# Kernel tuning notes

Hardware: AMD Instinct MI355X
Metric: run time of the kernel (lower is better)

The kernel has to match this reference:

```python
import jax, jax.numpy as jnp
import numpy as np

B, S, H = 32, 1024, 512
D = 2 * H  # feature dim used by all projections


def setup_inputs() -> dict:
    key = jax.random.key(0)
    ks = jax.random.split(key, 8)
    sc = 1.0 / np.sqrt(D)
    return {
        "h_dec": jax.random.normal(ks[0], (1, B, H), jnp.float32),
        "c_dec": jax.random.normal(ks[1], (1, B, H), jnp.float32),
        "encoder_output": jax.random.normal(ks[2], (B, S, D), jnp.float32),
        "x_padding_masks": jnp.ones((B, S), jnp.float32),
        "coverage_vector": jnp.zeros((B, S), jnp.float32),
        "Wh_w": jax.random.normal(ks[3], (D, D), jnp.float32) * sc,
        "Ws_w": jax.random.normal(ks[4], (D, D), jnp.float32) * sc,
        "Ws_b": jax.random.normal(ks[5], (D,), jnp.float32) * sc,
        "Wc_w": jax.random.normal(ks[6], (D, 1), jnp.float32) * sc,
        "v_w": jax.random.normal(ks[7], (1, D), jnp.float32) * sc,
    }


def reference(h_dec, c_dec, encoder_output, x_padding_masks, coverage_vector,
              Wh_w, Ws_w, Ws_b, Wc_w, v_w):
    # s_t: (B, 1, 2H) -- decoder state, broadcast over seq instead of expand
    s_t = jnp.concatenate([h_dec, c_dec], axis=-1).transpose(1, 0, 2)
    dec_feat = s_t @ Ws_w.T + Ws_b                                  # (B,1,D)
    enc_feat = jnp.einsum('bsd,ed->bse', encoder_output, Wh_w)      # (B,S,D)
    cov_feat = coverage_vector[..., None] * Wc_w[:, 0]              # (B,S,D)
    atten_inputs = enc_feat + dec_feat + cov_feat
    score = jnp.einsum('bsd,d->bs', atten_inputs, v_w[0])           # (B,S)
    w = jax.nn.softmax(score, axis=1) * x_padding_masks
    w = w / jnp.sum(w, axis=1, keepdims=True)                       # renormalize
    context = jnp.einsum('bs,bsd->bd', w, encoder_output)           # (B,2H)
    coverage_new = coverage_vector + w
    return context, w, coverage_new
```

## Files before the change

kernel.cpp:

```cpp
#include <hip/hip_runtime.h>
#include <math.h>

#define B 32
#define S 1024
#define D 1024
#define NCHUNK 32
#define CROWS (S / NCHUNK)
#define WROWS (CROWS / 4)
#define THR 10.0f

#define WS_U      0
#define WS_CSC    1024
#define WS_SCORE  2048
#define WS_ML     (WS_SCORE + B * S)
#define WS_CTX    (WS_ML + B * NCHUNK * 2)

__global__ __launch_bounds__(256) void prep_kernel(
    const float* __restrict__ Wh, const float* __restrict__ Wc,
    const float* __restrict__ v, float* __restrict__ ws) {
    int blk = blockIdx.x, tid = threadIdx.x;
    if (blk == 128) {
        float p = 0.f;
        #pragma unroll
        for (int k = 0; k < 4; ++k) { int i = tid + k * 256; p += v[i] * Wc[i]; }
        __shared__ float red[256];
        red[tid] = p; __syncthreads();
        for (int s = 128; s > 0; s >>= 1) {
            if (tid < s) red[tid] += red[tid + s];
            __syncthreads();
        }
        if (tid == 0) ws[WS_CSC] = red[0];
        return;
    }
    int dchunk = blk >> 5, echunk = blk & 31;
    int d = dchunk * 256 + tid, e0 = echunk * 32;
    float acc = 0.f;
    #pragma unroll 8
    for (int e = e0; e < e0 + 32; ++e)
        acc += v[e] * Wh[e * D + d];
    atomicAdd(&ws[WS_U + d], acc);
}

__global__ __launch_bounds__(256) void fused_kernel(
    const float4* __restrict__ enc4, const float* __restrict__ cov,
    const float* __restrict__ mask, float* __restrict__ ws) {
    int chunk = blockIdx.x, b = blockIdx.y;
    int tid = threadIdx.x, wave = tid >> 6, lane = tid & 63;

    __shared__ float lds_ctx[4][D];
    __shared__ float lds_ml[4][2];

    const float4* u4 = (const float4*)(ws + WS_U);
    float4 uv0 = u4[lane * 4 + 0], uv1 = u4[lane * 4 + 1];
    float4 uv2 = u4[lane * 4 + 2], uv3 = u4[lane * 4 + 3];
    float cscale = ws[WS_CSC];

    float m = -INFINITY, l = 0.f;
    float4 c0 = make_float4(0, 0, 0, 0), c1 = c0, c2 = c0, c3 = c0;

    int s_base = chunk * CROWS + wave * WROWS;
    for (int r = 0; r < WROWS; r += 2) {
        int idxA = b * S + s_base + r;
        int idxB = idxA + 1;
        size_t roA = (size_t)idxA * 256 + lane * 4;
        size_t roB = (size_t)idxB * 256 + lane * 4;
        float4 a0 = enc4[roA + 0], a1 = enc4[roA + 1], a2 = enc4[roA + 2], a3 = enc4[roA + 3];
        float4 b0 = enc4[roB + 0], b1 = enc4[roB + 1], b2 = enc4[roB + 2], b3 = enc4[roB + 3];
        float accA = a0.x * uv0.x + a0.y * uv0.y + a0.z * uv0.z + a0.w * uv0.w
                   + a1.x * uv1.x + a1.y * uv1.y + a1.z * uv1.z + a1.w * uv1.w
                   + a2.x * uv2.x + a2.y * uv2.y + a2.z * uv2.z + a2.w * uv2.w
                   + a3.x * uv3.x + a3.y * uv3.y + a3.z * uv3.z + a3.w * uv3.w;
        float accB = b0.x * uv0.x + b0.y * uv0.y + b0.z * uv0.z + b0.w * uv0.w
                   + b1.x * uv1.x + b1.y * uv1.y + b1.z * uv1.z + b1.w * uv1.w
                   + b2.x * uv2.x + b2.y * uv2.y + b2.z * uv2.z + b2.w * uv2.w
                   + b3.x * uv3.x + b3.y * uv3.y + b3.z * uv3.z + b3.w * uv3.w;
        #pragma unroll
        for (int off = 32; off > 0; off >>= 1) {
            accA += __shfl_xor(accA, off, 64);
            accB += __shfl_xor(accB, off, 64);
        }
        float scA = accA + cov[idxA] * cscale;
        float scB = accB + cov[idxB] * cscale;
        if (lane == 0) {
            ws[WS_SCORE + idxA] = scA;
            ws[WS_SCORE + idxB] = scB;
        }
        float mx = fmaxf(scA, scB);
        if (mx > m + THR) {
            float scl = __expf(m - mx);
            l *= scl;
            c0.x *= scl; c0.y *= scl; c0.z *= scl; c0.w *= scl;
            c1.x *= scl; c1.y *= scl; c1.z *= scl; c1.w *= scl;
            c2.x *= scl; c2.y *= scl; c2.z *= scl; c2.w *= scl;
            c3.x *= scl; c3.y *= scl; c3.z *= scl; c3.w *= scl;
            m = mx;
        }
        float eA = __expf(scA - m) * mask[idxA];
        float eB = __expf(scB - m) * mask[idxB];
        l += eA + eB;
        c0.x += eA * a0.x + eB * b0.x; c0.y += eA * a0.y + eB * b0.y;
        c0.z += eA * a0.z + eB * b0.z; c0.w += eA * a0.w + eB * b0.w;
        c1.x += eA * a1.x + eB * b1.x; c1.y += eA * a1.y + eB * b1.y;
        c1.z += eA * a1.z + eB * b1.z; c1.w += eA * a1.w + eB * b1.w;
        c2.x += eA * a2.x + eB * b2.x; c2.y += eA * a2.y + eB * b2.y;
        c2.z += eA * a2.z + eB * b2.z; c2.w += eA * a2.w + eB * b2.w;
        c3.x += eA * a3.x + eB * b3.x; c3.y += eA * a3.y + eB * b3.y;
        c3.z += eA * a3.z + eB * b3.z; c3.w += eA * a3.w + eB * b3.w;
    }

    {
        float4* lc = (float4*)lds_ctx[wave];
        lc[lane * 4 + 0] = c0; lc[lane * 4 + 1] = c1;
        lc[lane * 4 + 2] = c2; lc[lane * 4 + 3] = c3;
        if (lane == 0) { lds_ml[wave][0] = m; lds_ml[wave][1] = l; }
    }
    __syncthreads();
    {
        float m0 = lds_ml[0][0], m1 = lds_ml[1][0], m2 = lds_ml[2][0], m3 = lds_ml[3][0];
        float mc = fmaxf(fmaxf(m0, m1), fmaxf(m2, m3));
        float f0 = __expf(m0 - mc), f1 = __expf(m1 - mc);
        float f2 = __expf(m2 - mc), f3 = __expf(m3 - mc);
        float lc = lds_ml[0][1] * f0 + lds_ml[1][1] * f1 + lds_ml[2][1] * f2 + lds_ml[3][1] * f3;
        float4 t0 = ((float4*)lds_ctx[0])[tid];
        float4 t1 = ((float4*)lds_ctx[1])[tid];
        float4 t2 = ((float4*)lds_ctx[2])[tid];
        float4 t3 = ((float4*)lds_ctx[3])[tid];
        float4 a;
        a.x = f0 * t0.x + f1 * t1.x + f2 * t2.x + f3 * t3.x;
        a.y = f0 * t0.y + f1 * t1.y + f2 * t2.y + f3 * t3.y;
        a.z = f0 * t0.z + f1 * t1.z + f2 * t2.z + f3 * t3.z;
        a.w = f0 * t0.w + f1 * t1.w + f2 * t2.w + f3 * t3.w;
        ((float4*)(ws + WS_CTX))[(b * NCHUNK + chunk) * 256 + tid] = a;
        if (tid == 0) {
            ws[WS_ML + (b * NCHUNK + chunk) * 2 + 0] = mc;
            ws[WS_ML + (b * NCHUNK + chunk) * 2 + 1] = lc;
        }
    }
}

__global__ __launch_bounds__(256) void finalize_kernel(
    const float* __restrict__ mask, const float* __restrict__ cov,
    const float* __restrict__ ws, float* __restrict__ out) {
    int part = blockIdx.x, b = blockIdx.y, tid = threadIdx.x;
    const float* ml = ws + WS_ML + b * NCHUNK * 2;
    float m_g = -INFINITY;
    #pragma unroll 8
    for (int c = 0; c < NCHUNK; ++c) m_g = fmaxf(m_g, ml[2 * c]);
    float l_g = 0.f;
    #pragma unroll 8
    for (int c = 0; c < NCHUNK; ++c) l_g += __expf(ml[2 * c] - m_g) * ml[2 * c + 1];
    float inv = 1.0f / l_g;

    if (part < 4) {
        int d = part * 256 + tid;
        float a = 0.f;
        #pragma unroll 8
        for (int c = 0; c < NCHUNK; ++c)
            a += __expf(ml[2 * c] - m_g) * ws[WS_CTX + (size_t)(b * NCHUNK + c) * D + d];
        out[b * D + d] = a * inv;
    } else {
        #pragma unroll
        for (int k = 0; k < 4; ++k) {
            int idx = b * S + tid + k * 256;
            float w = __expf(ws[WS_SCORE + idx] - m_g) * mask[idx] * inv;
            out[B * D + idx] = w;
            out[2 * B * D + idx] = cov[idx] + w;
        }
    }
}

extern "C" void kernel_launch(void* const* d_in, const int* in_sizes, int n_in,
                              void* d_out, int out_size, void* d_ws, size_t ws_size,
                              hipStream_t stream) {
    const float* enc   = (const float*)d_in[2];
    const float* mask  = (const float*)d_in[3];
    const float* cov   = (const float*)d_in[4];
    const float* Wh    = (const float*)d_in[5];
    const float* Wc    = (const float*)d_in[8];
    const float* v     = (const float*)d_in[9];
    float* out = (float*)d_out;
    float* ws  = (float*)d_ws;

    hipMemsetAsync(ws, 0, D * sizeof(float), stream);

    prep_kernel<<<129, 256, 0, stream>>>(Wh, Wc, v, ws);
    fused_kernel<<<dim3(NCHUNK, B), 256, 0, stream>>>(
        (const float4*)enc, cov, mask, ws);
    finalize_kernel<<<dim3(5, B), 256, 0, stream>>>(mask, cov, ws, out);
}
```

Before: 41.64 us.

## Coalesce encoder row loads and software-prefetch next row pair in fused kernel

Lanes now read the encoder row in an interleaved float4 layout (lane + k*64), so each wave load instruction covers a contiguous span. The u vector and the LDS context layout are remapped to match. The row loop is fully unrolled and double-buffered, so the next two rows are loaded while the current pair is reduced and accumulated, and cov and mask loads are hoisted earlier. The aim is better memory coalescing and hidden global load latency, at the cost of more registers, which may lower occupancy.

New measurement: 41.89 us. About the same (+0.6%).

```diff
diff --git a/kernel.cpp b/kernel.cpp
--- a/kernel.cpp
+++ b/kernel.cpp
@@ -51,36 +51,57 @@
     __shared__ float lds_ml[4][2];
 
     const float4* u4 = (const float4*)(ws + WS_U);
-    float4 uv0 = u4[lane * 4 + 0], uv1 = u4[lane * 4 + 1];
-    float4 uv2 = u4[lane * 4 + 2], uv3 = u4[lane * 4 + 3];
+    float4 uv0 = u4[0 * 64 + lane], uv1 = u4[1 * 64 + lane];
+    float4 uv2 = u4[2 * 64 + lane], uv3 = u4[3 * 64 + lane];
     float cscale = ws[WS_CSC];
 
     float m = -INFINITY, l = 0.f;
     float4 c0 = make_float4(0, 0, 0, 0), c1 = c0, c2 = c0, c3 = c0;
 
-    int s_base = chunk * CROWS + wave * WROWS;
+    int row0 = b * S + chunk * CROWS + wave * WROWS;
+
+    float4 A[2][4];
+    #pragma unroll
+    for (int j = 0; j < 2; ++j) {
+        size_t ro = (size_t)(row0 + j) * 256 + lane;
+        #pragma unroll
+        for (int k = 0; k < 4; ++k) A[j][k] = enc4[ro + k * 64];
+    }
+
+    #pragma unroll
     for (int r = 0; r < WROWS; r += 2) {
-        int idxA = b * S + s_base + r;
-        int idxB = idxA + 1;
-        size_t roA = (size_t)idxA * 256 + lane * 4;
-        size_t roB = (size_t)idxB * 256 + lane * 4;
-        float4 a0 = enc4[roA + 0], a1 = enc4[roA + 1], a2 = enc4[roA + 2], a3 = enc4[roA + 3];
-        float4 b0 = enc4[roB + 0], b1 = enc4[roB + 1], b2 = enc4[roB + 2], b3 = enc4[roB + 3];
-        float accA = a0.x * uv0.x + a0.y * uv0.y + a0.z * uv0.z + a0.w * uv0.w
-                   + a1.x * uv1.x + a1.y * uv1.y + a1.z * uv1.z + a1.w * uv1.w
-                   + a2.x * uv2.x + a2.y * uv2.y + a2.z * uv2.z + a2.w * uv2.w
-                   + a3.x * uv3.x + a3.y * uv3.y + a3.z * uv3.z + a3.w * uv3.w;
-        float accB = b0.x * uv0.x + b0.y * uv0.y + b0.z * uv0.z + b0.w * uv0.w
-                   + b1.x * uv1.x + b1.y * uv1.y + b1.z * uv1.z + b1.w * uv1.w
-                   + b2.x * uv2.x + b2.y * uv2.y + b2.z * uv2.z + b2.w * uv2.w
-                   + b3.x * uv3.x + b3.y * uv3.y + b3.z * uv3.z + b3.w * uv3.w;
+        int idxA = row0 + r, idxB = idxA + 1;
+        float cvA = cov[idxA], cvB = cov[idxB];
+        float mkA = mask[idxA], mkB = mask[idxB];
+
+        float4 Nx[2][4];
+        if (r + 2 < WROWS) {
+            #pragma unroll
+            for (int j = 0; j < 2; ++j) {
+                size_t ro = (size_t)(idxA + 2 + j) * 256 + lane;
+                #pragma unroll
+                for (int k = 0; k < 4; ++k) Nx[j][k] = enc4[ro + k * 64];
+            }
+        }
+
+        float pA0 = A[0][0].x * uv0.x + A[0][0].y * uv0.y + A[0][0].z * uv0.z + A[0][0].w * uv0.w;
+        float pA1 = A[0][1].x * uv1.x + A[0][1].y * uv1.y + A[0][1].z * uv1.z + A[0][1].w * uv1.w;
+        float pA2 = A[0][2].x * uv2.x + A[0][2].y * uv2.y + A[0][2].z * uv2.z + A[0][2].w * uv2.w;
+        float pA3 = A[0][3].x * uv3.x + A[0][3].y * uv3.y + A[0][3].z * uv3.z + A[0][3].w * uv3.w;
+        float pB0 = A[1][0].x * uv0.x + A[1][0].y * uv0.y + A[1][0].z * uv0.z + A[1][0].w * uv0.w;
+        float pB1 = A[1][1].x * uv1.x + A[1][1].y * uv1.y + A[1][1].z * uv1.z + A[1][1].w * uv1.w;
+        float pB2 = A[1][2].x * uv2.x + A[1][2].y * uv2.y + A[1][2].z * uv2.z + A[1][2].w * uv2.w;
+        float pB3 = A[1][3].x * uv3.x + A[1][3].y * uv3.y + A[1][3].z * uv3.z + A[1][3].w * uv3.w;
+        float accA = (pA0 + pA1) + (pA2 + pA3);
+        float accB = (pB0 + pB1) + (pB2 + pB3);
+
         #pragma unroll
         for (int off = 32; off > 0; off >>= 1) {
             accA += __shfl_xor(accA, off, 64);
             accB += __shfl_xor(accB, off, 64);
         }
-        float scA = accA + cov[idxA] * cscale;
-        float scB = accB + cov[idxB] * cscale;
+        float scA = accA + cvA * cscale;
+        float scB = accB + cvB * cscale;
         if (lane == 0) {
             ws[WS_SCORE + idxA] = scA;
             ws[WS_SCORE + idxB] = scB;
@@ -95,23 +116,30 @@
             c3.x *= scl; c3.y *= scl; c3.z *= scl; c3.w *= scl;
             m = mx;
         }
-        float eA = __expf(scA - m) * mask[idxA];
-        float eB = __expf(scB - m) * mask[idxB];
+        float eA = __expf(scA - m) * mkA;
+        float eB = __expf(scB - m) * mkB;
         l += eA + eB;
-        c0.x += eA * a0.x + eB * b0.x; c0.y += eA * a0.y + eB * b0.y;
-        c0.z += eA * a0.z + eB * b0.z; c0.w += eA * a0.w + eB * b0.w;
-        c1.x += eA * a1.x + eB * b1.x; c1.y += eA * a1.y + eB * b1.y;
-        c1.z += eA * a1.z + eB * b1.z; c1.w += eA * a1.w + eB * b1.w;
-        c2.x += eA * a2.x + eB * b2.x; c2.y += eA * a2.y + eB * b2.y;
-        c2.z += eA * a2.z + eB * b2.z; c2.w += eA * a2.w + eB * b2.w;
-        c3.x += eA * a3.x + eB * b3.x; c3.y += eA * a3.y + eB * b3.y;
-        c3.z += eA * a3.z + eB * b3.z; c3.w += eA * a3.w + eB * b3.w;
+        c0.x += eA * A[0][0].x + eB * A[1][0].x; c0.y += eA * A[0][0].y + eB * A[1][0].y;
+        c0.z += eA * A[0][0].z + eB * A[1][0].z; c0.w += eA * A[0][0].w + eB * A[1][0].w;
+        c1.x += eA * A[0][1].x + eB * A[1][1].x; c1.y += eA * A[0][1].y + eB * A[1][1].y;
+        c1.z += eA * A[0][1].z + eB * A[1][1].z; c1.w += eA * A[0][1].w + eB * A[1][1].w;
+        c2.x += eA * A[0][2].x + eB * A[1][2].x; c2.y += eA * A[0][2].y + eB * A[1][2].y;
+        c2.z += eA * A[0][2].z + eB * A[1][2].z; c2.w += eA * A[0][2].w + eB * A[1][2].w;
+        c3.x += eA * A[0][3].x + eB * A[1][3].x; c3.y += eA * A[0][3].y + eB * A[1][3].y;
+        c3.z += eA * A[0][3].z + eB * A[1][3].z; c3.w += eA * A[0][3].w + eB * A[1][3].w;
+
+        if (r + 2 < WROWS) {
+            #pragma unroll
+            for (int j = 0; j < 2; ++j)
+                #pragma unroll
+                for (int k = 0; k < 4; ++k) A[j][k] = Nx[j][k];
+        }
     }
 
     {
         float4* lc = (float4*)lds_ctx[wave];
-        lc[lane * 4 + 0] = c0; lc[lane * 4 + 1] = c1;
-        lc[lane * 4 + 2] = c2; lc[lane * 4 + 3] = c3;
+        lc[0 * 64 + lane] = c0; lc[1 * 64 + lane] = c1;
+        lc[2 * 64 + lane] = c2; lc[3 * 64 + lane] = c3;
         if (lane == 0) { lds_ml[wave][0] = m; lds_ml[wave][1] = l; }
     }
     __syncthreads();
```
